# Kernel tuning notes

Measured on AMD Instinct MI355X. Metric: run time of the kernel, lower is better.

## Reference

```python
import jax, jax.numpy as jnp
import numpy as np

HP = 64  # padded height (next pow2 of 56)
WP = 64  # padded width
H, W = 56, 56


def fwht(x):
    """Walsh-Hadamard transform along last axis (n must be power of 2)."""
    n = x.shape[-1]
    h = 1
    while h < n:
        xr = x.reshape(*x.shape[:-1], n // (2 * h), 2 * h)
        a = xr[..., :h]
        b = xr[..., h:]
        x = jnp.concatenate([a + b, a - b], axis=-1).reshape(*x.shape[:-1], n)
        h *= 2
    return x


def fwht_axis(x, axis):
    if axis == -1:
        return fwht(x)
    return jnp.swapaxes(fwht(jnp.swapaxes(x, -1, axis)), -1, axis)


def ifwht_axis(x, axis):
    n = x.shape[axis]
    return fwht_axis(x, axis) / n


def setup_inputs() -> dict:
    key = jax.random.key(0)
    k1, k2, k3, k4 = jax.random.split(key, 4)
    x = jax.random.normal(k1, (64, 128, H, W), dtype=jnp.float32)
    # per-pod 1x1 conv weights (pods, out_ch, in_ch), kaiming-ish scale
    conv_w = jax.random.normal(k2, (2, 128, 128), dtype=jnp.float32) / np.sqrt(128.0)
    v = jax.random.uniform(k3, (2, HP, WP), dtype=jnp.float32)
    T = jax.random.uniform(k4, (2, HP, WP), dtype=jnp.float32) / 10.0
    return {"x": x, "conv_w": conv_w, "v": v, "T": T}


def reference(x, conv_w, v, T):
    # pad spatial dims to power of 2 (pad right/bottom)
    f0 = jnp.pad(x, ((0, 0), (0, 0), (0, HP - H), (0, WP - W)))
    # 2D WHT
    f1 = fwht_axis(f0, -1)
    f2 = fwht_axis(f1, -2)
    # per-pod: elementwise gate v, 1x1 conv, soft-threshold; then sum over pods
    # f3: (P, B, Cin, HP, WP)
    f3 = v[:, None, None, :, :] * f2[None]
    f4 = jnp.einsum('pbihw,poi->pbohw', f3, conv_w)
    thr = jax.nn.relu(T)[:, None, None, :, :]
    f5 = jnp.sign(f4) * jax.nn.relu(jnp.abs(f4) - thr)
    f6 = f5.sum(axis=0)
    # inverse 2D WHT
    f7 = ifwht_axis(f6, -1)
    f8 = ifwht_axis(f7, -2)
    y = f8[..., :H, :W]
    return y + x  # residual
```

## Files before the change

kernel.cpp:

```cpp
#include <hip/hip_runtime.h>

typedef unsigned short u16;
typedef unsigned int u32;
typedef __attribute__((ext_vector_type(8))) __bf16 bf16x8;
typedef __attribute__((ext_vector_type(8))) unsigned short u16x8;
typedef __attribute__((ext_vector_type(2))) unsigned int u32x2;
typedef __attribute__((ext_vector_type(4))) float f32x4;

__device__ __forceinline__ u16 f2bf(float f) {
  u32 u = __builtin_bit_cast(u32, f);
  u += 0x7FFFu + ((u >> 16) & 1u);
  return (u16)(u >> 16);
}
__device__ __forceinline__ float bf2f(u16 h) {
  u32 u = ((u32)h) << 16;
  return __builtin_bit_cast(float, u);
}

template <int M>
__device__ __forceinline__ void bfly16(float r[16]) {
#pragma unroll
  for (int j = 0; j < 16; ++j)
    if ((j & M) == 0) {
      float a = r[j], b = r[j | M];
      r[j] = a + b;
      r[j | M] = a - b;
    }
}

__global__ __launch_bounds__(256) void k0_wcat(const float* __restrict__ cw,
                                               u16* __restrict__ wc) {
  const int i = blockIdx.x * 256 + threadIdx.x;
  const int j = i & 7;
  const int lr = (i >> 3) & 15;
  const int lq = (i >> 7) & 3;
  const int q = (i >> 9) & 3;
  const int fm = (i >> 11) & 1;
  const int wv = (i >> 12) & 3;
  const int fp = (i >> 14) & 1;
  const int row = fp * 128 + wv * 32 + fm * 16 + lr;
  const int k = q * 32 + lq * 8 + j;
  wc[i] = f2bf(cw[row * 128 + k]);
}

__global__ __launch_bounds__(256) void k1_fwht(const float* __restrict__ x,
                                               u16* __restrict__ f2) {
  __shared__ float lds[64 * 68];
  const int t = threadIdx.x;
  const int b = blockIdx.x >> 4;
  const int cg = blockIdx.x & 15;
  const int hA = t >> 2, wq = t & 3;
  const int hg = t >> 4, rB = t & 15;
  const int wC = t & 63, rr = t >> 6;
  const bool hok = hA < 56;
  u16x8 outv[16];

#pragma unroll
  for (int pp = 0; pp < 8; ++pp) {
    const float* xp = x + (size_t)(b * 128 + cg * 8 + pp) * 3136;
    float r[16];
#pragma unroll
    for (int c4 = 0; c4 < 4; ++c4) {
      const int w0 = wq * 16 + c4 * 4;
      if (hok && w0 < 56) {
        const float4 v4 = *(const float4*)(xp + hA * 56 + w0);
        r[c4 * 4 + 0] = v4.x; r[c4 * 4 + 1] = v4.y;
        r[c4 * 4 + 2] = v4.z; r[c4 * 4 + 3] = v4.w;
      } else {
        r[c4 * 4 + 0] = 0.f; r[c4 * 4 + 1] = 0.f;
        r[c4 * 4 + 2] = 0.f; r[c4 * 4 + 3] = 0.f;
      }
    }
    bfly16<1>(r); bfly16<2>(r); bfly16<4>(r); bfly16<8>(r);
    if (pp) __syncthreads();
#pragma unroll
    for (int c4 = 0; c4 < 4; ++c4)
      *(float4*)&lds[hA * 68 + wq * 16 + c4 * 4] =
          make_float4(r[c4 * 4 + 0], r[c4 * 4 + 1], r[c4 * 4 + 2], r[c4 * 4 + 3]);
    __syncthreads();
    float q[16];
#pragma unroll
    for (int k = 0; k < 4; ++k)
#pragma unroll
      for (int d = 0; d < 4; ++d)
        q[k * 4 + d] = lds[(hg * 4 + d) * 68 + k * 16 + rB];
    bfly16<4>(q); bfly16<8>(q); bfly16<1>(q); bfly16<2>(q);
#pragma unroll
    for (int k = 0; k < 4; ++k)
#pragma unroll
      for (int d = 0; d < 4; ++d)
        lds[(hg * 4 + d) * 68 + k * 16 + rB] = q[k * 4 + d];
    __syncthreads();
    float s[16];
#pragma unroll
    for (int j = 0; j < 16; ++j) s[j] = lds[(4 * j + rr) * 68 + wC];
    bfly16<1>(s); bfly16<2>(s); bfly16<4>(s); bfly16<8>(s);
#pragma unroll
    for (int j = 0; j < 16; ++j) outv[j][pp] = f2bf(s[j]);
  }
  u16* dst = f2 + ((size_t)(b * 16 + cg) << 15);
#pragma unroll
  for (int j = 0; j < 16; ++j) {
    const int pos = (4 * j + rr) * 64 + wC;
    *(u16x8*)(dst + (size_t)pos * 8) = outv[j];
  }
}

__global__ __launch_bounds__(256, 2) void k2_mix(u16* __restrict__ fg,
                                                 const u16* __restrict__ wc,
                                                 const float* __restrict__ vv,
                                                 const float* __restrict__ tt) {
  const int t = threadIdx.x;
  const int b = blockIdx.x >> 6;
  const int p0 = (blockIdx.x & 63) << 6;
  u16* fb = fg + ((size_t)b << 19);
  const int wv = t >> 6, l = t & 63, lr = l & 15, lq = l >> 4;

  bf16x8 bfr[4][4];
#pragma unroll
  for (int q = 0; q < 4; ++q)
#pragma unroll
    for (int fn = 0; fn < 4; ++fn)
      bfr[q][fn] = __builtin_bit_cast(
          bf16x8, *(const u16x8*)(fb + ((size_t)(4 * q + lq) << 15) +
                                  (size_t)(p0 + fn * 16 + lr) * 8));
  bf16x8 afr[4][2][2];
#pragma unroll
  for (int q = 0; q < 4; ++q)
#pragma unroll
    for (int fp = 0; fp < 2; ++fp)
#pragma unroll
      for (int fm = 0; fm < 2; ++fm) {
        const int frag_id = ((fp * 4 + wv) * 2 + fm) * 4 + q;
        afr[q][fp][fm] = __builtin_bit_cast(
            bf16x8, *(const u16x8*)(wc + (frag_id << 9) + l * 8));
      }
  float v0s[4], v1s[4], t0s[4], t1s[4];
#pragma unroll
  for (int fn = 0; fn < 4; ++fn) {
    const int pos = p0 + fn * 16 + lr;
    v0s[fn] = vv[pos];
    v1s[fn] = vv[4096 + pos];
    t0s[fn] = fmaxf(tt[pos], 0.f);
    t1s[fn] = fmaxf(tt[4096 + pos], 0.f);
  }

  f32x4 acc[2][2][4] = {};
#pragma unroll
  for (int q = 0; q < 4; ++q)
#pragma unroll
    for (int fn = 0; fn < 4; ++fn)
#pragma unroll
      for (int fp = 0; fp < 2; ++fp)
#pragma unroll
        for (int fm = 0; fm < 2; ++fm)
          acc[fp][fm][fn] = __builtin_amdgcn_mfma_f32_16x16x32_bf16(
              afr[q][fp][fm], bfr[q][fn], acc[fp][fm][fn], 0, 0, 0);

  __syncthreads();
#pragma unroll
  for (int fn = 0; fn < 4; ++fn) {
    const int pos = p0 + fn * 16 + lr;
#pragma unroll
    for (int fm = 0; fm < 2; ++fm) {
      u16 w[4];
#pragma unroll
      for (int rg = 0; rg < 4; ++rg) {
        const float z0 = v0s[fn] * acc[0][fm][fn][rg];
        const float z1 = v1s[fn] * acc[1][fm][fn][rg];
        const float s0v = copysignf(fmaxf(fabsf(z0) - t0s[fn], 0.f), z0);
        const float s1v = copysignf(fmaxf(fabsf(z1) - t1s[fn], 0.f), z1);
        w[rg] = f2bf(s0v + s1v);
      }
      const int og = wv * 4 + fm * 2 + (lq >> 1);
      u32x2 pk;
      pk[0] = (u32)w[0] | ((u32)w[1] << 16);
      pk[1] = (u32)w[2] | ((u32)w[3] << 16);
      *(u32x2*)(fb + ((size_t)og << 15) + (size_t)pos * 8 + (lq & 1) * 4) = pk;
    }
  }
}

__global__ __launch_bounds__(256) void k3_iwht(const u16* __restrict__ g,
                                               const float* __restrict__ x,
                                               float* __restrict__ y) {
  __shared__ float lds[64 * 68];
  const int t = threadIdx.x;
  const int b = blockIdx.x >> 4;
  const int og = blockIdx.x & 15;
  const u16* gb = g + ((size_t)(b * 16 + og) << 15);
  const int hA = t >> 2, wq = t & 3;
  const int hg = t >> 4, rB = t & 15;
  const int wC = t & 63, rr = t >> 6;
  u16x8 inv[16];
#pragma unroll
  for (int e = 0; e < 16; ++e)
    inv[e] = *(const u16x8*)(gb + (size_t)(hA * 64 + wq * 16 + e) * 8);

#pragma unroll
  for (int pp = 0; pp < 8; ++pp) {
    float r[16];
#pragma unroll
    for (int e = 0; e < 16; ++e) r[e] = bf2f(inv[e][pp]);
    bfly16<1>(r); bfly16<2>(r); bfly16<4>(r); bfly16<8>(r);
    if (pp) __syncthreads();
#pragma unroll
    for (int c4 = 0; c4 < 4; ++c4)
      *(float4*)&lds[hA * 68 + wq * 16 + c4 * 4] =
          make_float4(r[c4 * 4 + 0], r[c4 * 4 + 1], r[c4 * 4 + 2], r[c4 * 4 + 3]);
    __syncthreads();
    float q[16];
#pragma unroll
    for (int k = 0; k < 4; ++k)
#pragma unroll
      for (int d = 0; d < 4; ++d)
        q[k * 4 + d] = lds[(hg * 4 + d) * 68 + k * 16 + rB];
    bfly16<4>(q); bfly16<8>(q); bfly16<1>(q); bfly16<2>(q);
#pragma unroll
    for (int k = 0; k < 4; ++k)
#pragma unroll
      for (int d = 0; d < 4; ++d)
        lds[(hg * 4 + d) * 68 + k * 16 + rB] = q[k * 4 + d];
    __syncthreads();
    float s[16];
#pragma unroll
    for (int j = 0; j < 16; ++j) s[j] = lds[(4 * j + rr) * 68 + wC];
    bfly16<1>(s); bfly16<2>(s); bfly16<4>(s); bfly16<8>(s);
    if (wC < 56) {
      const size_t plane = (size_t)(b * 128 + og * 8 + pp) * 3136;
#pragma unroll
      for (int j = 0; j < 14; ++j) {
        const int h = 4 * j + rr;
        const size_t idx = plane + (size_t)(h * 56 + wC);
        y[idx] = x[idx] + s[j] * (1.f / 4096.f);
      }
    }
  }
}

extern "C" void kernel_launch(void* const* d_in, const int* in_sizes, int n_in,
                              void* d_out, int out_size, void* d_ws, size_t ws_size,
                              hipStream_t stream) {
  const float* x = (const float*)d_in[0];
  const float* cw = (const float*)d_in[1];
  const float* v = (const float*)d_in[2];
  const float* T = (const float*)d_in[3];
  float* y = (float*)d_out;

  u16* f2 = (u16*)d_ws;
  u16* wcat = (u16*)((char*)d_ws + 67108864);

  k0_wcat<<<128, 256, 0, stream>>>(cw, wcat);
  k1_fwht<<<1024, 256, 0, stream>>>(x, f2);
  k2_mix<<<4096, 256, 0, stream>>>(f2, wcat, v, T);
  k3_iwht<<<1024, 256, 0, stream>>>(f2, x, y);
}
```

Baseline: 124.6 us.

## Use DPP cross-lane butterflies in forward WHT and double-buffer LDS

The forward WHT kernel now finishes the last two butterfly stages of each 64-point row pass with DPP quad-permute exchanges across the four lanes that share a row, which removes the intermediate LDS transpose pass and one of its barriers. The LDS buffer is double-buffered by plane parity, so the barrier before each write is dropped as well. Each plane now needs a single __syncthreads instead of three. The cost is extra DPP moves and FMAs, a second LDS buffer, and a different column read pattern that may raise bank conflicts.

```diff
diff --git a/kernel.cpp b/kernel.cpp
--- a/kernel.cpp
+++ b/kernel.cpp
@@ -15,6 +15,18 @@
 __device__ __forceinline__ float bf2f(u16 h) {
   u32 u = ((u32)h) << 16;
   return __builtin_bit_cast(float, u);
+}
+
+template <int CTRL>
+__device__ __forceinline__ float dppf(float x) {
+  const int i = __builtin_bit_cast(int, x);
+  const int p = __builtin_amdgcn_update_dpp(i, i, CTRL, 0xF, 0xF, false);
+  return __builtin_bit_cast(float, p);
+}
+template <int CTRL>
+__device__ __forceinline__ void xstage16(float r[16], float sgn) {
+#pragma unroll
+  for (int i = 0; i < 16; ++i) r[i] = fmaf(sgn, r[i], dppf<CTRL>(r[i]));
 }
 
 template <int M>
@@ -45,64 +57,52 @@
 
 __global__ __launch_bounds__(256) void k1_fwht(const float* __restrict__ x,
                                                u16* __restrict__ f2) {
-  __shared__ float lds[64 * 68];
+  __shared__ float lds[2][64 * 68];
   const int t = threadIdx.x;
   const int b = blockIdx.x >> 4;
   const int cg = blockIdx.x & 15;
   const int hA = t >> 2, wq = t & 3;
-  const int hg = t >> 4, rB = t & 15;
-  const int wC = t & 63, rr = t >> 6;
+  const int wC = t >> 2, hq = t & 3;
   const bool hok = hA < 56;
+  const float sg1 = (t & 1) ? -1.f : 1.f;
+  const float sg2 = (t & 2) ? -1.f : 1.f;
+  const float* xbase = x + (size_t)(b * 128 + cg * 8) * 3136;
   u16x8 outv[16];
 
 #pragma unroll
   for (int pp = 0; pp < 8; ++pp) {
-    const float* xp = x + (size_t)(b * 128 + cg * 8 + pp) * 3136;
+    const float* xp = xbase + (size_t)pp * 3136;
     float r[16];
 #pragma unroll
     for (int c4 = 0; c4 < 4; ++c4) {
       const int w0 = wq * 16 + c4 * 4;
-      if (hok && w0 < 56) {
-        const float4 v4 = *(const float4*)(xp + hA * 56 + w0);
-        r[c4 * 4 + 0] = v4.x; r[c4 * 4 + 1] = v4.y;
-        r[c4 * 4 + 2] = v4.z; r[c4 * 4 + 3] = v4.w;
-      } else {
-        r[c4 * 4 + 0] = 0.f; r[c4 * 4 + 1] = 0.f;
-        r[c4 * 4 + 2] = 0.f; r[c4 * 4 + 3] = 0.f;
-      }
+      float4 v4 = make_float4(0.f, 0.f, 0.f, 0.f);
+      if (hok && w0 < 56) v4 = *(const float4*)(xp + hA * 56 + w0);
+      r[c4 * 4 + 0] = v4.x; r[c4 * 4 + 1] = v4.y;
+      r[c4 * 4 + 2] = v4.z; r[c4 * 4 + 3] = v4.w;
     }
     bfly16<1>(r); bfly16<2>(r); bfly16<4>(r); bfly16<8>(r);
-    if (pp) __syncthreads();
+    xstage16<0xB1>(r, sg1);
+    xstage16<0x4E>(r, sg2);
 #pragma unroll
     for (int c4 = 0; c4 < 4; ++c4)
-      *(float4*)&lds[hA * 68 + wq * 16 + c4 * 4] =
+      *(float4*)&lds[pp & 1][hA * 68 + wq * 16 + c4 * 4] =
           make_float4(r[c4 * 4 + 0], r[c4 * 4 + 1], r[c4 * 4 + 2], r[c4 * 4 + 3]);
     __syncthreads();
-    float q[16];
-#pragma unroll
-    for (int k = 0; k < 4; ++k)
-#pragma unroll
-      for (int d = 0; d < 4; ++d)
-        q[k * 4 + d] = lds[(hg * 4 + d) * 68 + k * 16 + rB];
-    bfly16<4>(q); bfly16<8>(q); bfly16<1>(q); bfly16<2>(q);
-#pragma unroll
-    for (int k = 0; k < 4; ++k)
-#pragma unroll
-      for (int d = 0; d < 4; ++d)
-        lds[(hg * 4 + d) * 68 + k * 16 + rB] = q[k * 4 + d];
-    __syncthreads();
     float s[16];
 #pragma unroll
-    for (int j = 0; j < 16; ++j) s[j] = lds[(4 * j + rr) * 68 + wC];
+    for (int i = 0; i < 16; ++i) s[i] = lds[pp & 1][(hq * 16 + i) * 68 + wC];
     bfly16<1>(s); bfly16<2>(s); bfly16<4>(s); bfly16<8>(s);
-#pragma unroll
-    for (int j = 0; j < 16; ++j) outv[j][pp] = f2bf(s[j]);
+    xstage16<0xB1>(s, sg1);
+    xstage16<0x4E>(s, sg2);
+#pragma unroll
+    for (int i = 0; i < 16; ++i) outv[i][pp] = f2bf(s[i]);
   }
   u16* dst = f2 + ((size_t)(b * 16 + cg) << 15);
 #pragma unroll
-  for (int j = 0; j < 16; ++j) {
-    const int pos = (4 * j + rr) * 64 + wC;
-    *(u16x8*)(dst + (size_t)pos * 8) = outv[j];
+  for (int i = 0; i < 16; ++i) {
+    const int pos = (hq * 16 + i) * 64 + wC;
+    *(u16x8*)(dst + (size_t)pos * 8) = outv[i];
   }
 }
 
```

Result: slower. 150.0 us (+20.4%).
